# Kernel optimization log

Measured on AMD Instinct MI355X. Metric: run time of the kernel, lower is better.

## Reference

```python
import jax, jax.numpy as jnp
import numpy as np

HIDDEN = 1152
HEADS = 16
HEAD_DIM = HIDDEN // HEADS

def setup_inputs() -> dict:
    key = jax.random.key(0)
    ks = jax.random.split(key, 7)
    s = 1.0 / np.sqrt(HIDDEN)
    return {
        "x": jax.random.normal(ks[0], (16, 1024, HIDDEN), dtype=jnp.float32),
        "w_qkv": jax.random.normal(ks[1], (3 * HIDDEN, HIDDEN), dtype=jnp.float32) * s,
        "b_qkv": jax.random.normal(ks[2], (3 * HIDDEN,), dtype=jnp.float32) * 0.01,
        "q_gamma": jnp.ones((HEAD_DIM,), dtype=jnp.float32),
        "k_gamma": jnp.ones((HEAD_DIM,), dtype=jnp.float32),
        "w_proj": jax.random.normal(ks[3], (HIDDEN, HIDDEN), dtype=jnp.float32) * s,
        "b_proj": jax.random.normal(ks[4], (HIDDEN,), dtype=jnp.float32) * 0.01,
    }

def _rmsnorm(t, gamma):
    # normalize over last dim (head_dim); torch RMSNorm default eps = finfo(dtype).eps
    eps = jnp.asarray(jnp.finfo(t.dtype).eps, t.dtype)
    ms = jnp.mean(jnp.square(t), axis=-1, keepdims=True)
    return t * jax.lax.rsqrt(ms + eps) * gamma

def reference(x, w_qkv, b_qkv, q_gamma, k_gamma, w_proj, b_proj):
    B, S, H = x.shape
    qkv = x @ w_qkv.T + b_qkv                       # [B,S,3H]
    qkv = qkv.reshape(B, S, 3, HEADS, HEAD_DIM)
    qkv = jnp.transpose(qkv, (2, 0, 3, 1, 4))       # [3,B,nh,S,hd]
    q, k, v = qkv[0], qkv[1], qkv[2]
    q = _rmsnorm(q, q_gamma)
    k = _rmsnorm(k, k_gamma)
    scale = 1.0 / np.sqrt(HEAD_DIM)
    scores = jnp.einsum('bhqd,bhkd->bhqk', q, k) * scale
    probs = jax.nn.softmax(scores, axis=-1)
    out = jnp.einsum('bhqk,bhkd->bhqd', probs, v)   # [B,nh,S,hd]
    out = jnp.transpose(out, (0, 2, 1, 3)).reshape(B, S, H)
    return out @ w_proj.T + b_proj
```

## Files before the change

### kernel.cpp

```cpp
#include <hip/hip_runtime.h>

typedef _Float16 f16;
typedef _Float16 f16x8 __attribute__((ext_vector_type(8)));
typedef _Float16 f16x4 __attribute__((ext_vector_type(4)));
typedef float f32x4 __attribute__((ext_vector_type(4)));

__device__ __forceinline__ void gld16(const void* g, void* l) {
    __builtin_amdgcn_global_load_lds(
        (const __attribute__((address_space(1))) void*)g,
        (__attribute__((address_space(3))) void*)l,
        16, 0, 0);
}

__global__ __launch_bounds__(256) void f32_to_f16_vec(const float* __restrict__ in,
                                                      f16* __restrict__ out, long n4) {
    long i = (long)blockIdx.x * 256 + threadIdx.x;
    if (i < n4) {
        float4 v = ((const float4*)in)[i];
        f16x4 o = {(f16)v.x, (f16)v.y, (f16)v.z, (f16)v.w};
        ((f16x4*)out)[i] = o;
    }
}

__global__ __launch_bounds__(256) void gemm_bt(const f16* __restrict__ A,
                                               const f16* __restrict__ B,
                                               const float* __restrict__ bias,
                                               float* __restrict__ Cf,
                                               f16* __restrict__ Ch,
                                               int M, int N, int K) {
    constexpr int BK = 32;
    __shared__ f16 As[128 * BK];
    __shared__ f16 Bs[128 * BK];
    const int tid = threadIdx.x;
    const int w = tid >> 6;
    const int lane = tid & 63;
    const int quad = lane >> 4;
    const int l16 = lane & 15;

    const int nblk = N >> 7;
    const int mblk = M >> 7;
    const int id = blockIdx.x;
    const int xcd = id & 7;
    const int s = id >> 3;
    const int per_band = nblk * 8;
    const int t = s / per_band;
    const int r0 = s - t * per_band;
    const int n_blk = r0 >> 3;
    const int mr = r0 & 7;
    const int bands_per_xcd = mblk >> 6;
    const int m_blk = (xcd * bands_per_xcd + t) * 8 + mr;

    const long m0 = (long)m_blk * 128;
    const long n0 = (long)n_blk * 128;

    const int srow = lane >> 2;
    const int scol = (lane & 3) * 8;
    const f16* gA = A + (m0 + w * 32 + srow) * (long)K + scol;
    const f16* gB = B + (n0 + w * 32 + srow) * (long)K + scol;
    const int lb0 = __builtin_amdgcn_readfirstlane(w * 1024);
    const int lb1 = __builtin_amdgcn_readfirstlane(w * 1024 + 512);

    const int mw = (w >> 1) * 64;
    const int nw = (w & 1) * 64;

    f32x4 acc[4][4] = {};

    for (int k0 = 0; k0 < K; k0 += BK) {
        gld16(gA + k0, &As[lb0]);
        gld16(gA + (long)16 * K + k0, &As[lb1]);
        gld16(gB + k0, &Bs[lb0]);
        gld16(gB + (long)16 * K + k0, &Bs[lb1]);
        __syncthreads();
        f16x8 af[4], bf[4];
#pragma unroll
        for (int t2 = 0; t2 < 4; ++t2)
            af[t2] = *(const f16x8*)&As[(mw + t2 * 16 + l16) * BK + quad * 8];
#pragma unroll
        for (int t2 = 0; t2 < 4; ++t2)
            bf[t2] = *(const f16x8*)&Bs[(nw + t2 * 16 + l16) * BK + quad * 8];
#pragma unroll
        for (int mt = 0; mt < 4; ++mt)
#pragma unroll
            for (int nt = 0; nt < 4; ++nt)
                acc[mt][nt] = __builtin_amdgcn_mfma_f32_16x16x32_f16(
                    af[mt], bf[nt], acc[mt][nt], 0, 0, 0);
        __syncthreads();
    }

    float bv[4];
#pragma unroll
    for (int nt = 0; nt < 4; ++nt)
        bv[nt] = bias ? bias[n0 + nw + nt * 16 + l16] : 0.f;
#pragma unroll
    for (int mt = 0; mt < 4; ++mt) {
#pragma unroll
        for (int r = 0; r < 4; ++r) {
            const long row = m0 + mw + mt * 16 + quad * 4 + r;
#pragma unroll
            for (int nt = 0; nt < 4; ++nt) {
                const long col = n0 + nw + nt * 16 + l16;
                const float v = acc[mt][nt][r] + bv[nt];
                if (Ch) Ch[row * (long)N + col] = (f16)v;
                else    Cf[row * (long)N + col] = v;
            }
        }
    }
}

__global__ __launch_bounds__(256) void qk_norm2(f16* __restrict__ qkv,
                                                const float* __restrict__ qg,
                                                const float* __restrict__ kg,
                                                f16* __restrict__ kc) {
    const float QSCALE = 0.117851130198f;
    const int t = blockIdx.x * 256 + threadIdx.x;
    const int h = t & 15;
    const long bs = t >> 4;
    f16* qp = qkv + bs * 3456 + h * 72;
    {
        f16x8 v[9];
        float ss = 0.f;
#pragma unroll
        for (int c = 0; c < 9; ++c) {
            v[c] = *(const f16x8*)(qp + c * 8);
#pragma unroll
            for (int j = 0; j < 8; ++j) { float f = (float)v[c][j]; ss += f * f; }
        }
        const float rs = rsqrtf(ss * (1.f / 72.f) + 1.1920928955078125e-7f) * QSCALE;
#pragma unroll
        for (int c = 0; c < 9; ++c) {
            f16x8 o;
#pragma unroll
            for (int j = 0; j < 8; ++j) o[j] = (f16)((float)v[c][j] * rs * qg[c * 8 + j]);
            *(f16x8*)(qp + c * 8) = o;
        }
    }
    {
        const f16* kp = qp + 1152;
        f16* dst = kc + ((long)((bs >> 10) * 16 + h) * 1024 + (bs & 1023)) * 72;
        f16x8 v[9];
        float ss = 0.f;
#pragma unroll
        for (int c = 0; c < 9; ++c) {
            v[c] = *(const f16x8*)(kp + c * 8);
#pragma unroll
            for (int j = 0; j < 8; ++j) { float f = (float)v[c][j]; ss += f * f; }
        }
        const float rs = rsqrtf(ss * (1.f / 72.f) + 1.1920928955078125e-7f);
#pragma unroll
        for (int c = 0; c < 9; ++c) {
            f16x8 o;
#pragma unroll
            for (int j = 0; j < 8; ++j) o[j] = (f16)((float)v[c][j] * rs * kg[c * 8 + j]);
            *(f16x8*)(dst + c * 8) = o;
        }
    }
}

__global__ __launch_bounds__(256) void vt_kernel(const f16* __restrict__ QKV,
                                                 f16* __restrict__ Vt) {
    __shared__ f16 tile[64][73];
    const int tid = threadIdx.x;
    const int bh = blockIdx.x;
    const int b = bh >> 4, h = bh & 15;
    const int s0 = blockIdx.y * 64;
    for (int idx = tid; idx < 64 * 72; idx += 256) {
        const int r = idx / 72, c = idx % 72;
        tile[r][c] = QKV[((long)(b * 1024 + s0 + r)) * 3456 + 2304 + h * 72 + c];
    }
    __syncthreads();
    for (int idx = tid; idx < 72 * 64; idx += 256) {
        const int d = idx >> 6, s = idx & 63;
        Vt[((long)bh * 72 + d) * 1024 + s0 + s] = tile[s][d];
    }
}

__global__ __launch_bounds__(256) void attn2(const f16* __restrict__ QKV,
                                             const f16* __restrict__ Kc,
                                             const f16* __restrict__ Vt,
                                             f16* __restrict__ O) {
    constexpr int S = 1024;
    __shared__ f16 smem[64 * 72 + 80 * 76];
    f16* Ks = smem;
    f16* Vs = smem + 64 * 72;
    const int tid = threadIdx.x;
    const int w = tid >> 6, lane = tid & 63;
    const int quad = lane >> 4, l16 = lane & 15;

    const int b = blockIdx.x;
    const int xcd = b & 7;
    const int j = b >> 3;
    const int bh = ((j >> 3) << 3) | xcd;
    const int qt = j & 7;
    const int bb = bh >> 4, h = bh & 15;
    const int q0 = qt * 128;

    for (int i = tid; i < 8 * 76; i += 256) {
        const int pr = i / 76, pc = i % 76;
        Vs[(72 + pr) * 76 + pc] = (pr == 0 && pc < 64) ? (f16)1.f : (f16)0.f;
    }

    const f16* qrow0 = QKV + ((long)(bb * 1024 + q0 + w * 32 + l16)) * 3456 + h * 72;
    const f16* qrow1 = qrow0 + (long)16 * 3456;
    f16x8 qz = {};
    f16x8 qf[2][3];
    qf[0][0] = *(const f16x8*)(qrow0 + quad * 8);
    qf[0][1] = *(const f16x8*)(qrow0 + 32 + quad * 8);
    qf[0][2] = (quad == 0) ? *(const f16x8*)(qrow0 + 64) : qz;
    qf[1][0] = *(const f16x8*)(qrow1 + quad * 8);
    qf[1][1] = *(const f16x8*)(qrow1 + 32 + quad * 8);
    qf[1][2] = (quad == 0) ? *(const f16x8*)(qrow1 + 64) : qz;

    f32x4 o[2][5] = {};

    const f16* gK = Kc + (long)bh * S * 72;
    const f16* gV = Vt + (long)bh * 72 * S;

    for (int s0 = 0; s0 < S; s0 += 64) {
        for (int ch = w; ch < 9; ch += 4)
            gld16(gK + (long)s0 * 72 + ch * 512 + lane * 8,
                  &Ks[__builtin_amdgcn_readfirstlane(ch * 512)]);
#pragma unroll
        for (int it = 0; it < 3; ++it) {
            const int idx = it * 256 + tid;
            if (idx < 576) {
                const int d = idx >> 3, s8 = (idx & 7) * 8;
                f16x8 v = *(const f16x8*)(gV + (long)d * 1024 + s0 + s8);
                f16x4 lo = {v[0], v[1], v[2], v[3]};
                f16x4 hi = {v[4], v[5], v[6], v[7]};
                *(f16x4*)&Vs[d * 76 + s8] = lo;
                *(f16x4*)&Vs[d * 76 + s8 + 4] = hi;
            }
        }
        __syncthreads();

        f32x4 sc[4][2] = {};
#pragma unroll
        for (int ss = 0; ss < 4; ++ss) {
            const int base = (ss * 16 + l16) * 72;
            f16x8 k0 = *(const f16x8*)&Ks[base + quad * 8];
            f16x8 k1 = *(const f16x8*)&Ks[base + 32 + quad * 8];
            f16x8 k2 = *(const f16x8*)&Ks[base + 64 + quad * 8];
            sc[ss][0] = __builtin_amdgcn_mfma_f32_16x16x32_f16(k0, qf[0][0], sc[ss][0], 0, 0, 0);
            sc[ss][0] = __builtin_amdgcn_mfma_f32_16x16x32_f16(k1, qf[0][1], sc[ss][0], 0, 0, 0);
            sc[ss][0] = __builtin_amdgcn_mfma_f32_16x16x32_f16(k2, qf[0][2], sc[ss][0], 0, 0, 0);
            sc[ss][1] = __builtin_amdgcn_mfma_f32_16x16x32_f16(k0, qf[1][0], sc[ss][1], 0, 0, 0);
            sc[ss][1] = __builtin_amdgcn_mfma_f32_16x16x32_f16(k1, qf[1][1], sc[ss][1], 0, 0, 0);
            sc[ss][1] = __builtin_amdgcn_mfma_f32_16x16x32_f16(k2, qf[1][2], sc[ss][1], 0, 0, 0);
        }

        f16x4 pf[4][2];
#pragma unroll
        for (int ss = 0; ss < 4; ++ss)
#pragma unroll
            for (int qs = 0; qs < 2; ++qs) {
                f16x4 pk;
#pragma unroll
                for (int r = 0; r < 4; ++r) pk[r] = (f16)__expf(sc[ss][qs][r]);
                pf[ss][qs] = pk;
            }

#pragma unroll
        for (int vt = 0; vt < 5; ++vt) {
#pragma unroll
            for (int ss = 0; ss < 4; ++ss) {
                f16x4 vf = *(const f16x4*)&Vs[(vt * 16 + l16) * 76 + ss * 16 + quad * 4];
                o[0][vt] = __builtin_amdgcn_mfma_f32_16x16x16f16(vf, pf[ss][0], o[0][vt], 0, 0, 0);
                o[1][vt] = __builtin_amdgcn_mfma_f32_16x16x16f16(vf, pf[ss][1], o[1][vt], 0, 0, 0);
            }
        }
        __syncthreads();
    }

    const float l0 = __shfl(o[0][4][0], 32 + l16);
    const float l1 = __shfl(o[1][4][0], 32 + l16);
    const float inv[2] = {1.f / l0, 1.f / l1};

    f16* es = smem + w * 2560;
#pragma unroll
    for (int qs = 0; qs < 2; ++qs) {
        f16* row = es + (qs * 16 + l16) * 80;
#pragma unroll
        for (int vt = 0; vt < 5; ++vt)
#pragma unroll
            for (int r = 0; r < 4; ++r) {
                const int d = vt * 16 + quad * 4 + r;
                if (d < 72) row[d] = (f16)(o[qs][vt][r] * inv[qs]);
            }
    }
    const long rowbase = (long)bb * 1024 + q0 + w * 32;
#pragma unroll
    for (int it = 0; it < 5; ++it) {
        const int idx = it * 64 + lane;
        if (idx < 288) {
            const int q = idx / 9, c = idx - q * 9;
            f16x4 a = *(const f16x4*)&es[q * 80 + c * 8];
            f16x4 b2 = *(const f16x4*)&es[q * 80 + c * 8 + 4];
            f16* dst = O + (rowbase + q) * 1152 + h * 72 + c * 8;
            *(f16x4*)dst = a;
            *(f16x4*)(dst + 4) = b2;
        }
    }
}

extern "C" void kernel_launch(void* const* d_in, const int* in_sizes, int n_in,
                              void* d_out, int out_size, void* d_ws, size_t ws_size,
                              hipStream_t stream) {
    const float* x       = (const float*)d_in[0];
    const float* w_qkv   = (const float*)d_in[1];
    const float* b_qkv   = (const float*)d_in[2];
    const float* q_gamma = (const float*)d_in[3];
    const float* k_gamma = (const float*)d_in[4];
    const float* w_proj  = (const float*)d_in[5];
    const float* b_proj  = (const float*)d_in[6];
    float* out = (float*)d_out;

    char* p = (char*)d_ws;
    f16* x_h = (f16*)p;      p += (size_t)16384 * 1152 * 2;
    f16* wqkv_h = (f16*)p;   p += (size_t)3456 * 1152 * 2;
    f16* wproj_h = (f16*)p;  p += (size_t)1152 * 1152 * 2;
    f16* qkv_h = (f16*)p;    p += (size_t)16384 * 3456 * 2;
    const size_t needed = (size_t)(p - (char*)d_ws);
    if (ws_size < needed) return;

    f16* k_c = (f16*)d_out;
    f16* v_t = (f16*)d_out + (size_t)16384 * 1152;

    f32_to_f16_vec<<<18432, 256, 0, stream>>>(x, x_h, 16384L * 1152 / 4);
    f32_to_f16_vec<<<3888, 256, 0, stream>>>(w_qkv, wqkv_h, 3456L * 1152 / 4);
    f32_to_f16_vec<<<1296, 256, 0, stream>>>(w_proj, wproj_h, 1152L * 1152 / 4);

    gemm_bt<<<27 * 128, 256, 0, stream>>>(
        x_h, wqkv_h, b_qkv, nullptr, qkv_h, 16384, 3456, 1152);

    qk_norm2<<<1024, 256, 0, stream>>>(qkv_h, q_gamma, k_gamma, k_c);
    vt_kernel<<<dim3(256, 16), 256, 0, stream>>>(qkv_h, v_t);

    attn2<<<2048, 256, 0, stream>>>(qkv_h, k_c, v_t, x_h );

    gemm_bt<<<9 * 128, 256, 0, stream>>>(
        x_h, wproj_h, b_proj, out, nullptr, 16384, 1152, 1152);
}
```

Before: 584.1 us.

## Double-buffer K/V tiles in attention with async LDS loads and swizzled V layout

The V-transpose kernel now writes V in per-64-key tile blocks with an XOR swizzle, so each tile is contiguous and can be loaded straight into LDS with global_load_lds, just like K. The attention kernel double-buffers the K and V tiles and issues the next tile's loads before computing on the current one, which drops one barrier per iteration. The swizzled V reads are meant to avoid LDS bank conflicts now that the padding is gone. The cost is more LDS per block, which may lower occupancy.

```diff
diff --git a/kernel.cpp b/kernel.cpp
--- a/kernel.cpp
+++ b/kernel.cpp
@@ -157,46 +157,47 @@
 }
 
 __global__ __launch_bounds__(256) void vt_kernel(const f16* __restrict__ QKV,
-                                                 f16* __restrict__ Vt) {
+                                                 f16* __restrict__ Vt2) {
     __shared__ f16 tile[64][73];
     const int tid = threadIdx.x;
     const int bh = blockIdx.x;
     const int b = bh >> 4, h = bh & 15;
-    const int s0 = blockIdx.y * 64;
+    const int st = blockIdx.y;
+    const int s0 = st * 64;
     for (int idx = tid; idx < 64 * 72; idx += 256) {
         const int r = idx / 72, c = idx % 72;
         tile[r][c] = QKV[((long)(b * 1024 + s0 + r)) * 3456 + 2304 + h * 72 + c];
     }
     __syncthreads();
+    f16* dst = Vt2 + ((long)bh * 16 + st) * 4608;
     for (int idx = tid; idx < 72 * 64; idx += 256) {
         const int d = idx >> 6, s = idx & 63;
-        Vt[((long)bh * 72 + d) * 1024 + s0 + s] = tile[s][d];
-    }
-}
-
-__global__ __launch_bounds__(256) void attn2(const f16* __restrict__ QKV,
+        dst[d * 64 + (s ^ ((d & 7) << 3))] = tile[s][d];
+    }
+}
+
+__global__ __launch_bounds__(256) void attn3(const f16* __restrict__ QKV,
                                              const f16* __restrict__ Kc,
-                                             const f16* __restrict__ Vt,
+                                             const f16* __restrict__ Vt2,
                                              f16* __restrict__ O) {
     constexpr int S = 1024;
-    __shared__ f16 smem[64 * 72 + 80 * 76];
-    f16* Ks = smem;
-    f16* Vs = smem + 64 * 72;
+    __shared__ f16 smem[19456];
     const int tid = threadIdx.x;
     const int w = tid >> 6, lane = tid & 63;
     const int quad = lane >> 4, l16 = lane & 15;
-
-    const int b = blockIdx.x;
-    const int xcd = b & 7;
-    const int j = b >> 3;
+    const int swz = (l16 & 7) << 3;
+
+    const int bx = blockIdx.x;
+    const int xcd = bx & 7;
+    const int j = bx >> 3;
     const int bh = ((j >> 3) << 3) | xcd;
     const int qt = j & 7;
     const int bb = bh >> 4, h = bh & 15;
     const int q0 = qt * 128;
 
-    for (int i = tid; i < 8 * 76; i += 256) {
-        const int pr = i / 76, pc = i % 76;
-        Vs[(72 + pr) * 76 + pc] = (pr == 0 && pc < 64) ? (f16)1.f : (f16)0.f;
+    for (int i = tid; i < 2 * 8 * 64; i += 256) {
+        const int buf = i >> 9, r = (i >> 6) & 7, c = i & 63;
+        smem[9216 + buf * 5120 + (72 + r) * 64 + c] = (r == 0) ? (f16)1.f : (f16)0.f;
     }
 
     const f16* qrow0 = QKV + ((long)(bb * 1024 + q0 + w * 32 + l16)) * 3456 + h * 72;
@@ -213,33 +214,38 @@
     f32x4 o[2][5] = {};
 
     const f16* gK = Kc + (long)bh * S * 72;
-    const f16* gV = Vt + (long)bh * 72 * S;
-
-    for (int s0 = 0; s0 < S; s0 += 64) {
-        for (int ch = w; ch < 9; ch += 4)
-            gld16(gK + (long)s0 * 72 + ch * 512 + lane * 8,
-                  &Ks[__builtin_amdgcn_readfirstlane(ch * 512)]);
-#pragma unroll
-        for (int it = 0; it < 3; ++it) {
-            const int idx = it * 256 + tid;
-            if (idx < 576) {
-                const int d = idx >> 3, s8 = (idx & 7) * 8;
-                f16x8 v = *(const f16x8*)(gV + (long)d * 1024 + s0 + s8);
-                f16x4 lo = {v[0], v[1], v[2], v[3]};
-                f16x4 hi = {v[4], v[5], v[6], v[7]};
-                *(f16x4*)&Vs[d * 76 + s8] = lo;
-                *(f16x4*)&Vs[d * 76 + s8 + 4] = hi;
-            }
-        }
+    const f16* gV = Vt2 + (long)bh * 16 * 4608;
+
+    for (int ch = w; ch < 9; ch += 4) {
+        const int lb = __builtin_amdgcn_readfirstlane(ch * 512);
+        gld16(gK + ch * 512 + lane * 8, &smem[lb]);
+        gld16(gV + ch * 512 + lane * 8, &smem[9216 + lb]);
+    }
+
+    for (int t = 0; t < 16; ++t) {
         __syncthreads();
+        const int cur = t & 1;
+        const int ko = cur * 4608;
+        const int vo = 9216 + cur * 5120;
+        if (t < 15) {
+            const f16* gKn = gK + (t + 1) * 4608;
+            const f16* gVn = gV + (t + 1) * 4608;
+            const int kon = (cur ^ 1) * 4608;
+            const int von = 9216 + (cur ^ 1) * 5120;
+            for (int ch = w; ch < 9; ch += 4) {
+                const int lb = __builtin_amdgcn_readfirstlane(ch * 512);
+                gld16(gKn + ch * 512 + lane * 8, &smem[kon + lb]);
+                gld16(gVn + ch * 512 + lane * 8, &smem[von + lb]);
+            }
+        }
 
         f32x4 sc[4][2] = {};
 #pragma unroll
         for (int ss = 0; ss < 4; ++ss) {
-            const int base = (ss * 16 + l16) * 72;
-            f16x8 k0 = *(const f16x8*)&Ks[base + quad * 8];
-            f16x8 k1 = *(const f16x8*)&Ks[base + 32 + quad * 8];
-            f16x8 k2 = *(const f16x8*)&Ks[base + 64 + quad * 8];
+            const int base = ko + (ss * 16 + l16) * 72;
+            f16x8 k0 = *(const f16x8*)&smem[base + quad * 8];
+            f16x8 k1 = *(const f16x8*)&smem[base + 32 + quad * 8];
+            f16x8 k2 = *(const f16x8*)&smem[base + 64 + quad * 8];
             sc[ss][0] = __builtin_amdgcn_mfma_f32_16x16x32_f16(k0, qf[0][0], sc[ss][0], 0, 0, 0);
             sc[ss][0] = __builtin_amdgcn_mfma_f32_16x16x32_f16(k1, qf[0][1], sc[ss][0], 0, 0, 0);
             sc[ss][0] = __builtin_amdgcn_mfma_f32_16x16x32_f16(k2, qf[0][2], sc[ss][0], 0, 0, 0);
@@ -263,18 +269,18 @@
         for (int vt = 0; vt < 5; ++vt) {
 #pragma unroll
             for (int ss = 0; ss < 4; ++ss) {
-                f16x4 vf = *(const f16x4*)&Vs[(vt * 16 + l16) * 76 + ss * 16 + quad * 4];
+                f16x4 vf = *(const f16x4*)&smem[vo + (vt * 16 + l16) * 64 + ((ss * 16 + quad * 4) ^ swz)];
                 o[0][vt] = __builtin_amdgcn_mfma_f32_16x16x16f16(vf, pf[ss][0], o[0][vt], 0, 0, 0);
                 o[1][vt] = __builtin_amdgcn_mfma_f32_16x16x16f16(vf, pf[ss][1], o[1][vt], 0, 0, 0);
             }
         }
-        __syncthreads();
     }
 
     const float l0 = __shfl(o[0][4][0], 32 + l16);
     const float l1 = __shfl(o[1][4][0], 32 + l16);
     const float inv[2] = {1.f / l0, 1.f / l1};
 
+    __syncthreads();
     f16* es = smem + w * 2560;
 #pragma unroll
     for (int qs = 0; qs < 2; ++qs) {
@@ -323,7 +329,7 @@
     if (ws_size < needed) return;
 
     f16* k_c = (f16*)d_out;
-    f16* v_t = (f16*)d_out + (size_t)16384 * 1152;
+    f16* v_t2 = (f16*)d_out + (size_t)16384 * 1152;
 
     f32_to_f16_vec<<<18432, 256, 0, stream>>>(x, x_h, 16384L * 1152 / 4);
     f32_to_f16_vec<<<3888, 256, 0, stream>>>(w_qkv, wqkv_h, 3456L * 1152 / 4);
@@ -333,9 +339,9 @@
         x_h, wqkv_h, b_qkv, nullptr, qkv_h, 16384, 3456, 1152);
 
     qk_norm2<<<1024, 256, 0, stream>>>(qkv_h, q_gamma, k_gamma, k_c);
-    vt_kernel<<<dim3(256, 16), 256, 0, stream>>>(qkv_h, v_t);
-
-    attn2<<<2048, 256, 0, stream>>>(qkv_h, k_c, v_t, x_h );
+    vt_kernel<<<dim3(256, 16), 256, 0, stream>>>(qkv_h, v_t2);
+
+    attn3<<<2048, 256, 0, stream>>>(qkv_h, k_c, v_t2, x_h );
 
     gemm_bt<<<9 * 128, 256, 0, stream>>>(
         x_h, wproj_h, b_proj, out, nullptr, 16384, 1152, 1152);
```

New measurement: 597.2 us. 1.02x slower.
